# Kernel optimization log

Hardware: AMD Instinct MI355X
Metric: run time of the kernel (lower is better)

Reference implementation:

```python
import jax, jax.numpy as jnp
import numpy as np

B, H, D = 32, 64, 128          # batch (decode), indexer heads, head dim
PAGE, PAGES = 64, 128          # cache page size, pages per sequence
S = PAGE * PAGES               # max kv len = 8192
NUM_PAGES = B * PAGES          # 4096 pages total
TOPK = 2048
SCALE = float(D) ** -0.5
FILL = -1


def setup_inputs() -> dict:
    key = jax.random.key(0)
    ks = jax.random.split(key, 6)
    q = jax.random.normal(ks[0], (B, H, D), dtype=jnp.float32)
    k = jax.random.normal(ks[1], (B, D), dtype=jnp.float32)          # current-step key
    weights = jax.random.uniform(ks[2], (B, H), dtype=jnp.float32)   # per-head gates
    # fp8 cache emulated as quantized values (k_cache) x per-token scales (k_s_cache)
    k_cache = jax.random.normal(ks[3], (NUM_PAGES, PAGE, D), dtype=jnp.float32)
    k_s_cache = jax.random.uniform(ks[4], (NUM_PAGES, PAGE), minval=0.5, maxval=1.5, dtype=jnp.float32)
    kv_seqlens = jax.random.randint(ks[5], (B,), S // 2, S + 1, dtype=jnp.int32)
    block_offsets = jnp.arange(NUM_PAGES, dtype=jnp.int32).reshape(B, PAGES)
    return dict(q=q, k=k, weights=weights, k_cache=k_cache, k_s_cache=k_s_cache,
                kv_seqlens=kv_seqlens, block_offsets=block_offsets)


def reference(q, k, weights, k_cache, k_s_cache, kv_seqlens, block_offsets):
    # Gather paged cache per sequence and dequantize: [B, S, D]
    kv = k_cache[block_offsets].reshape(B, S, D) * k_s_cache[block_offsets].reshape(B, S, 1)
    pos = jnp.arange(S, dtype=jnp.int32)
    # Current step's key lives at position kv_len - 1
    cur = pos[None, :] == (kv_seqlens[:, None] - 1)
    kv = jnp.where(cur[..., None], k[:, None, :], kv)
    # Indexer score: sum_h w[b,h] * relu(q[b,h] . k[b,s]) * scale
    logits = jnp.einsum('bhd,bsd->bhs', q, kv) * SCALE
    scores = jnp.einsum('bh,bhs->bs', weights, jax.nn.relu(logits))  # [B, S]
    valid = pos[None, :] < kv_seqlens[:, None]
    scores = jnp.where(valid, scores, -jnp.inf)
    vals, idx = jax.lax.top_k(scores, TOPK)
    idx = jnp.where(jnp.isfinite(vals), idx, FILL).astype(jnp.int32)
    return idx, scores
```

## Files before the change

kernel.cpp:

```cpp
#include <hip/hip_runtime.h>
#include <hip/hip_bf16.h>
#include <math.h>

#define NB 32
#define NH 64
#define ND 128
#define PAGE_SZ 64
#define NPAGES 128
#define NS 8192
#define NTOPK 2048
#define QSCALE 0.08838834764831845f
#define NEG_SENTINEL -3.0e38f

typedef __attribute__((ext_vector_type(8))) short short8;
typedef __attribute__((ext_vector_type(4))) float f32x4;

static __device__ __forceinline__ unsigned pack2(float x, float y) {
    union { __hip_bfloat162 h; unsigned u; } c;
    c.h = __float22bfloat162_rn(make_float2(x, y));
    return c.u;
}

static __device__ __forceinline__ short8 pack8(const float4 &a, const float4 &b) {
    union { unsigned u[4]; short8 s; } c;
    c.u[0] = pack2(a.x, a.y);
    c.u[1] = pack2(a.z, a.w);
    c.u[2] = pack2(b.x, b.y);
    c.u[3] = pack2(b.z, b.w);
    return c.s;
}

__global__ __launch_bounds__(256, 4) void score_kernel(
    const float* __restrict__ q,
    const float* __restrict__ kcur,
    const float* __restrict__ w,
    const float* __restrict__ kc,
    const float* __restrict__ ksc,
    const int*   __restrict__ kvlen,
    const int*   __restrict__ bo,
    float* __restrict__ scores_out)
{
    __shared__ __align__(16) unsigned short q_lds[64 * 128];
    __shared__ float w_lds[NH];

    const int b    = blockIdx.y;
    const int sb   = blockIdx.x;
    const int t    = threadIdx.x;
    const int wv   = t >> 6;
    const int lane = t & 63;
    const int len  = kvlen[b];
    const int cur  = len - 1;
    const int s_base = sb * 256;

    if (s_base >= len) {
        scores_out[(size_t)b * NS + s_base + t] = NEG_SENTINEL;
        return;
    }

    const int tok = wv * 16 + (lane & 15);
    const int l4  = lane >> 4;

    float4 gA[8];
    float  scA;

#define LOADP(P)                                                              \
    {                                                                         \
        int pg = bo[b * NPAGES + sb * 4 + (P)];                               \
        int tg = s_base + (P) * 64 + tok;                                     \
        bool iscur = (tg == cur);                                             \
        const float* kb = iscur ? (kcur + (size_t)b * ND)                     \
                                : (kc + (size_t)pg * (PAGE_SZ * ND) +         \
                                   (size_t)tok * ND);                         \
        scA = iscur ? 1.0f : ksc[pg * PAGE_SZ + tok];                         \
        _Pragma("unroll")                                                     \
        for (int ki = 0; ki < 4; ++ki) {                                      \
            gA[2 * ki]     = *(const float4*)(kb + ki * 32 + l4 * 8);         \
            gA[2 * ki + 1] = *(const float4*)(kb + ki * 32 + l4 * 8 + 4);     \
        }                                                                     \
    }

    LOADP(0)

    const float* qb = q + (size_t)b * NH * ND;
#pragma unroll
    for (int i = 0; i < 8; ++i) {
        int f = t + 256 * i;
        int row = f >> 5, d4 = f & 31;
        float4 v = *(const float4*)(qb + row * ND + d4 * 4);
        unsigned lo = pack2(v.x, v.y);
        unsigned hi = pack2(v.z, v.w);
        int ck = (d4 >> 1) ^ (row & 7);
        *(uint2*)(q_lds + row * 128 + (ck << 3) + (d4 & 1) * 4) = make_uint2(lo, hi);
    }
    if (t < NH) w_lds[t] = w[b * NH + t];
    __syncthreads();

    float wgt[4][4];
#pragma unroll
    for (int hb = 0; hb < 4; ++hb)
#pragma unroll
        for (int r = 0; r < 4; ++r)
            wgt[hb][r] = w_lds[hb * 16 + (lane >> 4) * 4 + r];

    const int arow = lane & 15;
    const int aswz = lane & 7;

#pragma unroll
    for (int p = 0; p < 4; ++p) {
        short8 bF[4];
#pragma unroll
        for (int ki = 0; ki < 4; ++ki) bF[ki] = pack8(gA[2 * ki], gA[2 * ki + 1]);
        const float scP = scA;

        if (p < 3) LOADP(p + 1)

        f32x4 acc[4];
#pragma unroll
        for (int hb = 0; hb < 4; ++hb) acc[hb] = (f32x4){0.f, 0.f, 0.f, 0.f};
#pragma unroll
        for (int ki = 0; ki < 4; ++ki) {
            const int ck = (ki * 4 + l4) ^ aswz;
#pragma unroll
            for (int hb = 0; hb < 4; ++hb) {
                short8 a = *(const short8*)(
                    q_lds + (hb * 16 + arow) * 128 + (ck << 3));
                acc[hb] = __builtin_amdgcn_mfma_f32_16x16x32_bf16(
                    a, bF[ki], acc[hb], 0, 0, 0);
            }
        }

        float part = 0.f;
#pragma unroll
        for (int hb = 0; hb < 4; ++hb)
#pragma unroll
            for (int r = 0; r < 4; ++r)
                part = fmaf(wgt[hb][r], fmaxf(acc[hb][r], 0.f), part);
        part += __shfl_xor(part, 16);
        part += __shfl_xor(part, 32);
        int sg = s_base + p * 64 + tok;
        if (l4 == 0) {
            float val = part * (scP * QSCALE);
            scores_out[(size_t)b * NS + sg] = (sg < len) ? val : NEG_SENTINEL;
        }
    }
#undef LOADP
}

static __device__ __forceinline__ void cex(unsigned &a, unsigned &b, bool desc) {
    unsigned lo = a < b ? a : b;
    unsigned hi = a < b ? b : a;
    a = desc ? hi : lo;
    b = desc ? lo : hi;
}

__global__ __launch_bounds__(256) void topk_sort(
    const float* __restrict__ scores,
    const int*   __restrict__ kvlen,
    unsigned* __restrict__ wsk)
{
    __shared__ unsigned keys[2048];
    const int b = blockIdx.y, c = blockIdx.x, t = threadIdx.x;
    unsigned* wrow = wsk + ((size_t)b * 4 + c) * 2048;

    if (c * 2048 >= kvlen[b]) {
#pragma unroll
        for (int r = 0; r < 8; ++r) wrow[t * 8 + r] = 0u;
        return;
    }

    const float* srow = scores + (size_t)b * NS + c * 2048;
    unsigned v[8];
    {
        float4 f0 = *(const float4*)(srow + t * 8);
        float4 f1 = *(const float4*)(srow + t * 8 + 4);
        float fv[8] = {f0.x, f0.y, f0.z, f0.w, f1.x, f1.y, f1.z, f1.w};
#pragma unroll
        for (int r = 0; r < 8; ++r) {
            int s = c * 2048 + t * 8 + r;
            float x = fv[r];
            v[r] = (x >= 0.f)
                 ? ((__float_as_uint(x) & 0xFFFFC000u) | (unsigned)(8192 - s))
                 : 0u;
        }
    }

    cex(v[0], v[1], true);  cex(v[2], v[3], false);
    cex(v[4], v[5], true);  cex(v[6], v[7], false);
    cex(v[0], v[2], true);  cex(v[1], v[3], true);
    cex(v[4], v[6], false); cex(v[5], v[7], false);
    cex(v[0], v[1], true);  cex(v[2], v[3], true);
    cex(v[4], v[5], false); cex(v[6], v[7], false);

    for (int k = 8; k <= 2048; k <<= 1) {
        const bool desc = (((unsigned)(t << 3)) & (unsigned)k) == 0u;
        for (int j = k >> 1; j >= 8; j >>= 1) {
            const int m = j >> 3;
            const bool keepHi = (((t & m) == 0) == desc);
            if (m < 64) {
#pragma unroll
                for (int r = 0; r < 8; ++r) {
                    unsigned o = __shfl_xor(v[r], m);
                    unsigned lo = v[r] < o ? v[r] : o;
                    unsigned hi = v[r] < o ? o : v[r];
                    v[r] = keepHi ? hi : lo;
                }
            } else {
                __syncthreads();
#pragma unroll
                for (int r = 0; r < 8; ++r) keys[t * 8 + r] = v[r];
                __syncthreads();
                const int pt = t ^ m;
#pragma unroll
                for (int r = 0; r < 8; ++r) {
                    unsigned o = keys[pt * 8 + r];
                    unsigned lo = v[r] < o ? v[r] : o;
                    unsigned hi = v[r] < o ? o : v[r];
                    v[r] = keepHi ? hi : lo;
                }
            }
        }
        cex(v[0], v[4], desc); cex(v[1], v[5], desc);
        cex(v[2], v[6], desc); cex(v[3], v[7], desc);
        cex(v[0], v[2], desc); cex(v[1], v[3], desc);
        cex(v[4], v[6], desc); cex(v[5], v[7], desc);
        cex(v[0], v[1], desc); cex(v[2], v[3], desc);
        cex(v[4], v[5], desc); cex(v[6], v[7], desc);
    }

#pragma unroll
    for (int r = 0; r < 8; ++r) wrow[t * 8 + r] = v[r];
}

__global__ __launch_bounds__(512) void topk_merge(
    const unsigned* __restrict__ wsk,
    int* __restrict__ idx_out)
{
    __shared__ unsigned keys[4096];
    const int b = blockIdx.x, t = threadIdx.x;
    const int g = t >> 8, tl = t & 255;
    const unsigned* base = wsk + (size_t)b * 4 * 2048;

    const unsigned* A = base + (2 * g) * 2048;
    const unsigned* B = base + (2 * g + 1) * 2048;
    unsigned v[8];
#pragma unroll
    for (int r = 0; r < 8; ++r) {
        int i = tl * 8 + r;
        unsigned a = A[i], bb = B[2047 - i];
        v[r] = a > bb ? a : bb;
    }
#pragma unroll
    for (int j = 1024; j >= 512; j >>= 1) {
        const int m = j >> 3;
        const bool keepHi = ((tl & m) == 0);
        __syncthreads();
#pragma unroll
        for (int r = 0; r < 8; ++r) keys[g * 2048 + tl * 8 + r] = v[r];
        __syncthreads();
        const int pt = tl ^ m;
#pragma unroll
        for (int r = 0; r < 8; ++r) {
            unsigned o = keys[g * 2048 + pt * 8 + r];
            unsigned lo = v[r] < o ? v[r] : o;
            unsigned hi = v[r] < o ? o : v[r];
            v[r] = keepHi ? hi : lo;
        }
    }
#pragma unroll
    for (int j = 256; j >= 8; j >>= 1) {
        const int m = j >> 3;
        const bool keepHi = ((tl & m) == 0);
#pragma unroll
        for (int r = 0; r < 8; ++r) {
            unsigned o = __shfl_xor(v[r], m);
            unsigned lo = v[r] < o ? v[r] : o;
            unsigned hi = v[r] < o ? o : v[r];
            v[r] = keepHi ? hi : lo;
        }
    }
    cex(v[0], v[4], true); cex(v[1], v[5], true);
    cex(v[2], v[6], true); cex(v[3], v[7], true);
    cex(v[0], v[2], true); cex(v[1], v[3], true);
    cex(v[4], v[6], true); cex(v[5], v[7], true);
    cex(v[0], v[1], true); cex(v[2], v[3], true);
    cex(v[4], v[5], true); cex(v[6], v[7], true);

    __syncthreads();
#pragma unroll
    for (int r = 0; r < 8; ++r) keys[g * 2048 + tl * 8 + r] = v[r];
    __syncthreads();

    unsigned u[4];
#pragma unroll
    for (int r = 0; r < 4; ++r) {
        int i = t * 4 + r;
        unsigned a = keys[i], bb = keys[2048 + 2047 - i];
        u[r] = a > bb ? a : bb;
    }
#pragma unroll
    for (int j = 1024; j >= 256; j >>= 1) {
        const int m = j >> 2;
        const bool keepHi = ((t & m) == 0);
        __syncthreads();
#pragma unroll
        for (int r = 0; r < 4; ++r) keys[t * 4 + r] = u[r];
        __syncthreads();
        const int pt = t ^ m;
#pragma unroll
        for (int r = 0; r < 4; ++r) {
            unsigned o = keys[pt * 4 + r];
            unsigned lo = u[r] < o ? u[r] : o;
            unsigned hi = u[r] < o ? o : u[r];
            u[r] = keepHi ? hi : lo;
        }
    }
#pragma unroll
    for (int j = 128; j >= 4; j >>= 1) {
        const int m = j >> 2;
        const bool keepHi = ((t & m) == 0);
#pragma unroll
        for (int r = 0; r < 4; ++r) {
            unsigned o = __shfl_xor(u[r], m);
            unsigned lo = u[r] < o ? u[r] : o;
            unsigned hi = u[r] < o ? o : u[r];
            u[r] = keepHi ? hi : lo;
        }
    }
    cex(u[0], u[2], true); cex(u[1], u[3], true);
    cex(u[0], u[1], true); cex(u[2], u[3], true);

#pragma unroll
    for (int r = 0; r < 4; ++r) {
        unsigned key = u[r];
        idx_out[b * NTOPK + t * 4 + r] =
            key ? (int)(8192u - (key & 0x3FFFu)) : -1;
    }
}

extern "C" void kernel_launch(void* const* d_in, const int* in_sizes, int n_in,
                              void* d_out, int out_size, void* d_ws, size_t ws_size,
                              hipStream_t stream)
{
    const float* q     = (const float*)d_in[0];
    const float* kcur  = (const float*)d_in[1];
    const float* w     = (const float*)d_in[2];
    const float* kc    = (const float*)d_in[3];
    const float* ksc   = (const float*)d_in[4];
    const int*   kvlen = (const int*)d_in[5];
    const int*   bo    = (const int*)d_in[6];

    int*      idx_out    = (int*)d_out;
    float*    scores_out = (float*)d_out + (size_t)NB * NTOPK;
    unsigned* wsk        = (unsigned*)d_ws;

    score_kernel<<<dim3(32, NB), 256, 0, stream>>>(q, kcur, w, kc, ksc, kvlen,
                                                   bo, scores_out);
    topk_sort<<<dim3(4, NB), 256, 0, stream>>>(scores_out, kvlen, wsk);
    topk_merge<<<NB, 512, 0, stream>>>(wsk, idx_out);
}
```

Baseline: 43.32 us.

## Assign one page per block and stage coalesced K tile through LDS

The score kernel now processes one 64-token page per block instead of four pages, which quadruples the grid to 128x32 blocks. Each block loads the whole page with fully coalesced float4 reads, converts it to bf16 and writes it to a swizzled LDS tile, and the MFMA B fragments are then read from LDS. This is meant to raise memory-level parallelism and coalescing. The cost is that every block reloads and repacks the full Q matrix, which is four times more Q traffic and packing work, and it adds 16KB of LDS per block, which may limit occupancy.

```diff
diff --git a/kernel.cpp b/kernel.cpp
--- a/kernel.cpp
+++ b/kernel.cpp
@@ -19,15 +19,6 @@
     union { __hip_bfloat162 h; unsigned u; } c;
     c.h = __float22bfloat162_rn(make_float2(x, y));
     return c.u;
-}
-
-static __device__ __forceinline__ short8 pack8(const float4 &a, const float4 &b) {
-    union { unsigned u[4]; short8 s; } c;
-    c.u[0] = pack2(a.x, a.y);
-    c.u[1] = pack2(a.z, a.w);
-    c.u[2] = pack2(b.x, b.y);
-    c.u[3] = pack2(b.z, b.w);
-    return c.s;
 }
 
 __global__ __launch_bounds__(256, 4) void score_kernel(
@@ -41,45 +32,41 @@
     float* __restrict__ scores_out)
 {
     __shared__ __align__(16) unsigned short q_lds[64 * 128];
+    __shared__ __align__(16) unsigned short kv_lds[64 * 128];
     __shared__ float w_lds[NH];
 
     const int b    = blockIdx.y;
-    const int sb   = blockIdx.x;
+    const int pi   = blockIdx.x;
     const int t    = threadIdx.x;
     const int wv   = t >> 6;
     const int lane = t & 63;
     const int len  = kvlen[b];
     const int cur  = len - 1;
-    const int s_base = sb * 256;
+    const int s_base = pi * 64;
 
     if (s_base >= len) {
-        scores_out[(size_t)b * NS + s_base + t] = NEG_SENTINEL;
+        if (t < 64)
+            scores_out[(size_t)b * NS + s_base + t] = NEG_SENTINEL;
         return;
     }
 
-    const int tok = wv * 16 + (lane & 15);
-    const int l4  = lane >> 4;
-
-    float4 gA[8];
-    float  scA;
-
-#define LOADP(P)                                                              \
-    {                                                                         \
-        int pg = bo[b * NPAGES + sb * 4 + (P)];                               \
-        int tg = s_base + (P) * 64 + tok;                                     \
-        bool iscur = (tg == cur);                                             \
-        const float* kb = iscur ? (kcur + (size_t)b * ND)                     \
-                                : (kc + (size_t)pg * (PAGE_SZ * ND) +         \
-                                   (size_t)tok * ND);                         \
-        scA = iscur ? 1.0f : ksc[pg * PAGE_SZ + tok];                         \
-        _Pragma("unroll")                                                     \
-        for (int ki = 0; ki < 4; ++ki) {                                      \
-            gA[2 * ki]     = *(const float4*)(kb + ki * 32 + l4 * 8);         \
-            gA[2 * ki + 1] = *(const float4*)(kb + ki * 32 + l4 * 8 + 4);     \
-        }                                                                     \
-    }
-
-    LOADP(0)
+    const int pg = bo[b * NPAGES + pi];
+    const float* kb = kc + (size_t)pg * (PAGE_SZ * ND);
+    float4 G[8];
+#pragma unroll
+    for (int i = 0; i < 8; ++i) {
+        int f   = t + 256 * i;
+        int tokL = f >> 5, d4 = f & 31;
+        bool iscur = (s_base + tokL) == cur;
+        const float* src = iscur ? (kcur + (size_t)b * ND + d4 * 4)
+                                 : (kb + (size_t)f * 4);
+        G[i] = *(const float4*)src;
+    }
+
+    const int tokP = wv * 16 + (lane & 15);
+    const int l4   = lane >> 4;
+    const bool curP = (s_base + tokP) == cur;
+    const float scP = curP ? 1.0f : ksc[pg * PAGE_SZ + tokP];
 
     const float* qb = q + (size_t)b * NH * ND;
 #pragma unroll
@@ -93,6 +80,17 @@
         *(uint2*)(q_lds + row * 128 + (ck << 3) + (d4 & 1) * 4) = make_uint2(lo, hi);
     }
     if (t < NH) w_lds[t] = w[b * NH + t];
+
+#pragma unroll
+    for (int i = 0; i < 8; ++i) {
+        int f = t + 256 * i;
+        int tokL = f >> 5, d4 = f & 31;
+        unsigned lo = pack2(G[i].x, G[i].y);
+        unsigned hi = pack2(G[i].z, G[i].w);
+        int ck = (d4 >> 1) ^ (tokL & 7);
+        *(uint2*)(kv_lds + tokL * 128 + (ck << 3) + (d4 & 1) * 4) = make_uint2(lo, hi);
+    }
+
     __syncthreads();
 
     float wgt[4][4];
@@ -100,50 +98,46 @@
     for (int hb = 0; hb < 4; ++hb)
 #pragma unroll
         for (int r = 0; r < 4; ++r)
-            wgt[hb][r] = w_lds[hb * 16 + (lane >> 4) * 4 + r];
+            wgt[hb][r] = w_lds[hb * 16 + l4 * 4 + r];
 
     const int arow = lane & 15;
     const int aswz = lane & 7;
 
-#pragma unroll
-    for (int p = 0; p < 4; ++p) {
-        short8 bF[4];
-#pragma unroll
-        for (int ki = 0; ki < 4; ++ki) bF[ki] = pack8(gA[2 * ki], gA[2 * ki + 1]);
-        const float scP = scA;
-
-        if (p < 3) LOADP(p + 1)
-
-        f32x4 acc[4];
-#pragma unroll
-        for (int hb = 0; hb < 4; ++hb) acc[hb] = (f32x4){0.f, 0.f, 0.f, 0.f};
-#pragma unroll
-        for (int ki = 0; ki < 4; ++ki) {
-            const int ck = (ki * 4 + l4) ^ aswz;
-#pragma unroll
-            for (int hb = 0; hb < 4; ++hb) {
-                short8 a = *(const short8*)(
-                    q_lds + (hb * 16 + arow) * 128 + (ck << 3));
-                acc[hb] = __builtin_amdgcn_mfma_f32_16x16x32_bf16(
-                    a, bF[ki], acc[hb], 0, 0, 0);
-            }
-        }
-
-        float part = 0.f;
-#pragma unroll
-        for (int hb = 0; hb < 4; ++hb)
-#pragma unroll
-            for (int r = 0; r < 4; ++r)
-                part = fmaf(wgt[hb][r], fmaxf(acc[hb][r], 0.f), part);
-        part += __shfl_xor(part, 16);
-        part += __shfl_xor(part, 32);
-        int sg = s_base + p * 64 + tok;
-        if (l4 == 0) {
-            float val = part * (scP * QSCALE);
-            scores_out[(size_t)b * NS + sg] = (sg < len) ? val : NEG_SENTINEL;
-        }
-    }
-#undef LOADP
+    short8 bF[4];
+#pragma unroll
+    for (int ki = 0; ki < 4; ++ki) {
+        int ch = (ki * 4 + l4) ^ (tokP & 7);
+        bF[ki] = *(const short8*)(kv_lds + tokP * 128 + (ch << 3));
+    }
+
+    f32x4 acc[4];
+#pragma unroll
+    for (int hb = 0; hb < 4; ++hb) acc[hb] = (f32x4){0.f, 0.f, 0.f, 0.f};
+#pragma unroll
+    for (int ki = 0; ki < 4; ++ki) {
+        const int ck = (ki * 4 + l4) ^ aswz;
+#pragma unroll
+        for (int hb = 0; hb < 4; ++hb) {
+            short8 a = *(const short8*)(
+                q_lds + (hb * 16 + arow) * 128 + (ck << 3));
+            acc[hb] = __builtin_amdgcn_mfma_f32_16x16x32_bf16(
+                a, bF[ki], acc[hb], 0, 0, 0);
+        }
+    }
+
+    float part = 0.f;
+#pragma unroll
+    for (int hb = 0; hb < 4; ++hb)
+#pragma unroll
+        for (int r = 0; r < 4; ++r)
+            part = fmaf(wgt[hb][r], fmaxf(acc[hb][r], 0.f), part);
+    part += __shfl_xor(part, 16);
+    part += __shfl_xor(part, 32);
+    int sg = s_base + tokP;
+    if (l4 == 0) {
+        float val = part * (scP * QSCALE);
+        scores_out[(size_t)b * NS + sg] = (sg < len) ? val : NEG_SENTINEL;
+    }
 }
 
 static __device__ __forceinline__ void cex(unsigned &a, unsigned &b, bool desc) {
@@ -353,8 +347,8 @@
     float*    scores_out = (float*)d_out + (size_t)NB * NTOPK;
     unsigned* wsk        = (unsigned*)d_ws;
 
-    score_kernel<<<dim3(32, NB), 256, 0, stream>>>(q, kcur, w, kc, ksc, kvlen,
-                                                   bo, scores_out);
+    score_kernel<<<dim3(128, NB), 256, 0, stream>>>(q, kcur, w, kc, ksc, kvlen,
+                                                    bo, scores_out);
     topk_sort<<<dim3(4, NB), 256, 0, stream>>>(scores_out, kvlen, wsk);
     topk_merge<<<NB, 512, 0, stream>>>(wsk, idx_out);
 }
```

Result: faster. 42.39 us (-2.1%).
